# Optimization experiments

Hardware: AMD Instinct MI355X
Metric: run time of the kernel (lower is better)

The kernel has to match this reference:

```python
import jax, jax.numpy as jnp
import numpy as np
import math

EMSIZE = 1024
B, S = 4, 1024
N = B * S

def setup_inputs() -> dict:
    key = jax.random.key(0)
    k1, k2, k3, k4, k5 = jax.random.split(key, 5)
    x = jax.random.normal(k1, (B, S, EMSIZE), dtype=jnp.float32)
    mask = jax.random.randint(k2, (N, N), 0, 2, dtype=jnp.int32)
    # nn.Linear default init scale ~ 1/sqrt(fan_in); use small normal weights
    sc = 1.0 / math.sqrt(EMSIZE)
    Wq = jax.random.normal(k3, (EMSIZE, EMSIZE), dtype=jnp.float32) * sc
    Wk = jax.random.normal(k4, (EMSIZE, EMSIZE), dtype=jnp.float32) * sc
    Wv = jax.random.normal(k5, (EMSIZE, EMSIZE), dtype=jnp.float32) * sc
    return {"x": x, "mask": mask, "Wq": Wq, "Wk": Wk, "Wv": Wv}

def reference(x, mask, Wq, Wk, Wv):
    b, s, e = x.shape
    xf = x.reshape(b * s, e)                       # [N, E]
    q = xf @ Wq.T                                  # nn.Linear: x @ W^T
    k = xf @ Wk.T
    v = xf @ Wv.T
    sim = q @ k.T                                  # [N, N] full cross-batch scores
    sim = jnp.where(mask == 0, jnp.float32(-1e20), sim)
    # NOTE: original scales AFTER masking, matching masked_fill then divide
    attn = jax.nn.softmax(sim / math.sqrt(e), axis=-1)
    out = attn @ v                                 # [N, E]
    return out.reshape(b, s, e)
```

## Files before the change

kernel.cpp:

```cpp
#include <hip/hip_runtime.h>
#include <hip/hip_bf16.h>
#include <math.h>


typedef __attribute__((ext_vector_type(8))) __bf16 bf16x8;
typedef __attribute__((ext_vector_type(4))) __bf16 bf16x4;
typedef __attribute__((ext_vector_type(4))) float f32x4;

__device__ __forceinline__ void gload_lds16(const void* g, void* l) {
  __builtin_amdgcn_global_load_lds(
      (__attribute__((address_space(1))) void*)(g),
      (__attribute__((address_space(3))) void*)(l), 16, 0, 0);
}

#define WAITB(N) asm volatile("s_waitcnt vmcnt(" #N ")\ns_barrier" ::: "memory")

#define LDS_FRAG(base, r) \
  *(const bf16x8*)((base) + (r) * 32 + (((hi) ^ (((r) >> 1) & 3)) * 8))

#define MM16(mq, AF)                                                        \
  __builtin_amdgcn_s_setprio(1);                                            \
  _Pragma("unroll") for (int m = 0; m < 4; ++m)                             \
    _Pragma("unroll") for (int n = 0; n < 4; ++n)                           \
      acc[(mq) * 4 + m][n] = __builtin_amdgcn_mfma_f32_16x16x32_bf16(       \
          AF[m], bfr[n], acc[(mq) * 4 + m][n], 0, 0, 0);                    \
  __builtin_amdgcn_s_setprio(0);

template <int NT>
__device__ __forceinline__ void g8_loop(const __bf16* __restrict__ A, long lda, long row0,
                                        const __bf16* __restrict__ B, long ldb, long col0,
                                        int kt0, __bf16* sA, __bf16* sB,
                                        f32x4 (&acc)[8][4], int tid) {
  const int lane = tid & 63;
  const int w = tid >> 6;
  const int wr = w >> 2, wc = w & 3;
  const int lo = lane & 15, hi = lane >> 4;

  auto stageA = [&](int buf, int kt) {
#pragma unroll
    for (int j = 0; j < 2; ++j) {
      int p = tid + j * 512;
      int row = p >> 2, cg = (p & 3) ^ ((row >> 1) & 3);
      gload_lds16(A + (row0 + row) * lda + kt * 32 + cg * 8,
                  sA + buf * 8192 + p * 8);
    }
  };
  auto stageB = [&](int buf, int kt) {
#pragma unroll
    for (int j = 0; j < 2; ++j) {
      int p = tid + j * 512;
      int row = p >> 2, cg = (p & 3) ^ ((row >> 1) & 3);
      gload_lds16(B + (col0 + row) * ldb + kt * 32 + cg * 8,
                  sB + buf * 8192 + p * 8);
    }
  };

#pragma unroll
  for (int t = 0; t < 3; ++t) { stageA(t, kt0 + t); stageB(t, kt0 + t); }
  WAITB(8);

  for (int t = 0; t < NT; ++t) {
    const int d = t & 3;
    const __bf16* sAc = sA + d * 8192;
    const __bf16* sBc = sB + d * 8192;
    const int s = (t + 3) & 3;
    bf16x8 af[4], bfr[4];
#pragma unroll
    for (int m = 0; m < 4; ++m) af[m] = LDS_FRAG(sAc, wr * 128 + m * 16 + lo);
#pragma unroll
    for (int n = 0; n < 4; ++n) bfr[n] = LDS_FRAG(sBc, wc * 64 + n * 16 + lo);
    if (t + 3 < NT) stageA(s, kt0 + t + 3);
    __builtin_amdgcn_s_barrier();
    MM16(0, af);
    __builtin_amdgcn_s_barrier();
    bf16x8 af2[4];
#pragma unroll
    for (int m = 0; m < 4; ++m) af2[m] = LDS_FRAG(sAc, wr * 128 + 64 + m * 16 + lo);
    if (t + 3 < NT) stageB(s, kt0 + t + 3);
    __builtin_amdgcn_s_barrier();
    MM16(1, af2);
    if (t + 3 < NT)      { WAITB(8); }
    else if (t + 2 < NT) { WAITB(4); }
    else                 { WAITB(0); }
  }
}


__global__ __launch_bounds__(512) void qkv8(const __bf16* __restrict__ xb,
                                            const __bf16* __restrict__ wq,
                                            const __bf16* __restrict__ wk,
                                            const __bf16* __restrict__ wv,
                                            __bf16* __restrict__ qb,
                                            __bf16* __restrict__ kb,
                                            __bf16* __restrict__ vtb) {
  __shared__ __bf16 sA[4 * 8192];
  __shared__ __bf16 sB[4 * 8192];
  const int raw = blockIdx.x;
  const int wid = (raw & 7) * 24 + (raw >> 3);
  const int z = wid >> 6;
  const int r2 = wid & 63;
  const int tid = threadIdx.x;
  const __bf16* A;
  const __bf16* B;
  long row0, col0;
  if (z == 2) {
    A = wv; B = xb;
    row0 = (long)(r2 >> 4) * 256;
    col0 = (long)(r2 & 15) * 256;
  } else {
    A = xb; B = (z == 0) ? wq : wk;
    row0 = (long)(r2 >> 2) * 256;
    col0 = (long)(r2 & 3) * 256;
  }
  f32x4 acc[8][4] = {};
  g8_loop<32>(A, 1024, row0, B, 1024, col0, 0, sA, sB, acc, tid);

  const int lane = tid & 63, w = tid >> 6;
  const int wr = w >> 2, wc = w & 3;
  const int lo = lane & 15, hi = lane >> 4;
#pragma unroll
  for (int m = 0; m < 8; ++m)
#pragma unroll
    for (int n = 0; n < 4; ++n)
#pragma unroll
      for (int i = 0; i < 4; ++i) {
        long r = row0 + wr * 128 + m * 16 + hi * 4 + i;
        long c = col0 + wc * 64 + n * 16 + lo;
        __bf16 v = (__bf16)acc[m][n][i];
        if (z == 0)      qb[r * 1024 + c] = v;
        else if (z == 1) kb[r * 1024 + c] = v;
        else             vtb[r * 4096 + c] = v;
      }
}

__global__ __launch_bounds__(512) void qk8(const __bf16* __restrict__ qb,
                                           const __bf16* __restrict__ kb,
                                           __bf16* __restrict__ sim) {
  __shared__ __bf16 sA[4 * 8192];
  __shared__ __bf16 sB[4 * 8192];
  const int raw = blockIdx.x;
  const int xcd = raw & 7, idx = raw >> 3;
  const int rp = (xcd >> 1) * 4 + (idx >> 3);
  const int cp = (xcd & 1) * 8 + (idx & 7);
  const long row0 = (long)rp * 256;
  const long col0 = (long)cp * 256;
  const int tid = threadIdx.x;
  f32x4 acc[8][4] = {};
  g8_loop<32>(qb, 1024, row0, kb, 1024, col0, 0, sA, sB, acc, tid);

  const int lane = tid & 63, w = tid >> 6;
  const int wr = w >> 2, wc = w & 3;
  const int lo = lane & 15, hi = lane >> 4;
#pragma unroll
  for (int m = 0; m < 8; ++m)
#pragma unroll
    for (int n = 0; n < 4; ++n)
#pragma unroll
      for (int i = 0; i < 4; ++i) {
        long r = row0 + wr * 128 + m * 16 + hi * 4 + i;
        long c = col0 + wc * 64 + n * 16 + lo;
        sim[r * 4096 + c] = (__bf16)acc[m][n][i];
      }
}

__global__ __launch_bounds__(256) void pv4(const __bf16* __restrict__ attn,
                                           const __bf16* __restrict__ vt,
                                           float* __restrict__ out) {
  __shared__ __bf16 sA[4 * 4096];
  __shared__ __bf16 sB[4 * 4096];
  const int raw = blockIdx.x;
  const int xcd = raw & 7, idx = raw >> 3;
  const int rp = (xcd >> 1) * 8 + (idx >> 2);
  const int cp = (xcd & 1) * 4 + (idx & 3);
  const long row0 = (long)rp * 128;
  const long col0 = (long)cp * 128;
  const int tid = threadIdx.x;
  const int lane = tid & 63, w = tid >> 6;
  const int wr = w >> 1, wc = w & 1;
  const int lo = lane & 15, hi = lane >> 4;
  constexpr int NT = 128;

  auto stageA = [&](int buf, int kt) {
#pragma unroll
    for (int j = 0; j < 2; ++j) {
      int p = tid + j * 256;
      int row = p >> 2, cg = (p & 3) ^ ((row >> 1) & 3);
      gload_lds16(attn + (row0 + row) * 4096 + kt * 32 + cg * 8,
                  sA + buf * 4096 + p * 8);
    }
  };
  auto stageB = [&](int buf, int kt) {
#pragma unroll
    for (int j = 0; j < 2; ++j) {
      int p = tid + j * 256;
      int row = p >> 2, cg = (p & 3) ^ ((row >> 1) & 3);
      gload_lds16(vt + (col0 + row) * 4096 + kt * 32 + cg * 8,
                  sB + buf * 4096 + p * 8);
    }
  };

  f32x4 acc[4][4] = {};
#pragma unroll
  for (int t = 0; t < 3; ++t) { stageA(t, t); stageB(t, t); }
  WAITB(8);

#pragma unroll 4
  for (int t = 0; t < NT; ++t) {
    const int d = t & 3;
    const __bf16* sAc = sA + d * 4096;
    const __bf16* sBc = sB + d * 4096;
    const int s = (t + 3) & 3;
    bf16x8 af[4], bfr[4];
#pragma unroll
    for (int m = 0; m < 4; ++m) af[m] = LDS_FRAG(sAc, wr * 64 + m * 16 + lo);
#pragma unroll
    for (int n = 0; n < 4; ++n) bfr[n] = LDS_FRAG(sBc, wc * 64 + n * 16 + lo);
    if (t + 3 < NT) { stageA(s, t + 3); stageB(s, t + 3); }
    __builtin_amdgcn_s_barrier();
    __builtin_amdgcn_s_setprio(1);
#pragma unroll
    for (int m = 0; m < 4; ++m)
#pragma unroll
      for (int n = 0; n < 4; ++n)
        acc[m][n] = __builtin_amdgcn_mfma_f32_16x16x32_bf16(af[m], bfr[n], acc[m][n], 0, 0, 0);
    __builtin_amdgcn_s_setprio(0);
    if (t + 3 < NT)      { WAITB(8); }
    else if (t + 2 < NT) { WAITB(4); }
    else                 { WAITB(0); }
  }

#pragma unroll
  for (int m = 0; m < 4; ++m)
#pragma unroll
    for (int n = 0; n < 4; ++n)
#pragma unroll
      for (int i = 0; i < 4; ++i) {
        long r = row0 + wr * 64 + m * 16 + hi * 4 + i;
        long c = col0 + wc * 64 + n * 16 + lo;
        out[r * 1024 + c] = acc[m][n][i];
      }
}

__global__ __launch_bounds__(256) void softmax_rows(__bf16* __restrict__ sim,
                                                    const int* __restrict__ mask) {
  const int row = blockIdx.x;
  __bf16* rp = sim + (size_t)row * 4096;
  const int4* mrow = (const int4*)(mask + (size_t)row * 4096);
  const int tid = threadIdx.x;

  float vals[16];
  float lmax = -INFINITY;
#pragma unroll
  for (int j = 0; j < 2; ++j) {
    bf16x8 s = ((const bf16x8*)rp)[tid + 256 * j];
    int4 m0 = mrow[(tid + 256 * j) * 2];
    int4 m1 = mrow[(tid + 256 * j) * 2 + 1];
    float f[8];
#pragma unroll
    for (int e = 0; e < 8; ++e) f[e] = (float)s[e];
    f[0] = m0.x ? f[0] : -1e20f;  f[1] = m0.y ? f[1] : -1e20f;
    f[2] = m0.z ? f[2] : -1e20f;  f[3] = m0.w ? f[3] : -1e20f;
    f[4] = m1.x ? f[4] : -1e20f;  f[5] = m1.y ? f[5] : -1e20f;
    f[6] = m1.z ? f[6] : -1e20f;  f[7] = m1.w ? f[7] : -1e20f;
#pragma unroll
    for (int e = 0; e < 8; ++e) {
      vals[8 * j + e] = f[e];
      lmax = fmaxf(lmax, f[e]);
    }
  }
#pragma unroll
  for (int off = 32; off; off >>= 1) lmax = fmaxf(lmax, __shfl_xor(lmax, off));
  __shared__ float red[4];
  __shared__ float bro[2];
  if ((tid & 63) == 0) red[tid >> 6] = lmax;
  __syncthreads();
  if (tid == 0) bro[0] = fmaxf(fmaxf(red[0], red[1]), fmaxf(red[2], red[3]));
  __syncthreads();
  const float m = bro[0];

  float e[16];
  float lsum = 0.f;
#pragma unroll
  for (int j = 0; j < 16; ++j) {
    e[j] = __expf((vals[j] - m) * 0.03125f);
    lsum += e[j];
  }
#pragma unroll
  for (int off = 32; off; off >>= 1) lsum += __shfl_xor(lsum, off);
  if ((tid & 63) == 0) red[tid >> 6] = lsum;
  __syncthreads();
  if (tid == 0) bro[1] = red[0] + red[1] + red[2] + red[3];
  __syncthreads();
  const float inv = 1.0f / bro[1];

#pragma unroll
  for (int j = 0; j < 2; ++j) {
    bf16x8 o;
#pragma unroll
    for (int q = 0; q < 8; ++q) o[q] = (__bf16)(e[8 * j + q] * inv);
    ((bf16x8*)rp)[tid + 256 * j] = o;
  }
}

__global__ __launch_bounds__(256) void cvt_all(const float* __restrict__ x,
                                               const float* __restrict__ wq,
                                               const float* __restrict__ wk,
                                               const float* __restrict__ wv,
                                               __bf16* __restrict__ xb,
                                               __bf16* __restrict__ wqb,
                                               __bf16* __restrict__ wkb,
                                               __bf16* __restrict__ wvb) {
  int b = blockIdx.x;
  const float* in;
  __bf16* out;
  int base;
  if (b < 4096)      { in = x;  out = xb;  base = b; }
  else if (b < 5120) { in = wq; out = wqb; base = b - 4096; }
  else if (b < 6144) { in = wk; out = wkb; base = b - 5120; }
  else               { in = wv; out = wvb; base = b - 6144; }
  int i = base * 256 + threadIdx.x;
  float4 f = ((const float4*)in)[i];
  bf16x4 o;
  o[0] = (__bf16)f.x; o[1] = (__bf16)f.y; o[2] = (__bf16)f.z; o[3] = (__bf16)f.w;
  ((bf16x4*)out)[i] = o;
}

extern "C" void kernel_launch(void* const* d_in, const int* in_sizes, int n_in,
                              void* d_out, int out_size, void* d_ws, size_t ws_size,
                              hipStream_t stream) {
  const float* x = (const float*)d_in[0];
  const int* mask = (const int*)d_in[1];
  const float* Wq = (const float*)d_in[2];
  const float* Wk = (const float*)d_in[3];
  const float* Wv = (const float*)d_in[4];
  float* out = (float*)d_out;

  char* ws = (char*)d_ws;
  __bf16* vtb = (__bf16*)(ws);
  __bf16* xb  = (__bf16*)(ws + (8ull << 20));
  __bf16* wqb = (__bf16*)(ws + (16ull << 20));
  __bf16* wkb = (__bf16*)(ws + (18ull << 20));
  __bf16* wvb = (__bf16*)(ws + (20ull << 20));
  __bf16* qb  = (__bf16*)(ws + (22ull << 20));
  __bf16* kb  = (__bf16*)(ws + (30ull << 20));
  __bf16* sim = (__bf16*)(ws + (38ull << 20));

  cvt_all<<<7168, 256, 0, stream>>>(x, Wq, Wk, Wv, xb, wqb, wkb, wvb);

  qkv8<<<192, 512, 0, stream>>>(xb, wqb, wkb, wvb, qb, kb, vtb);
  qk8<<<256, 512, 0, stream>>>(qb, kb, sim);
  softmax_rows<<<4096, 256, 0, stream>>>(sim, mask);
  pv4<<<256, 256, 0, stream>>>(sim, vtb, out);
}
```

Measured before the change: 155.4 us.

## Split-K the PV GEMM into two halves and add a reduction kernel

The attention-times-V GEMM now launches 512 blocks, each covering half of the 4096-long K dimension. One half writes into the output and the other into a workspace buffer, and a new float4 kernel then adds the two together. The aim is to fill more CUs on a machine with 256 CUs, where the old 256-block grid gave only one wave of blocks. The cost is an extra kernel launch plus 16 MB of fp32 partial-sum traffic. The QK block-to-XCD mapping is also changed, and the unroll pragma on the PV loop is removed.

```diff
diff --git a/kernel.cpp b/kernel.cpp
--- a/kernel.cpp
+++ b/kernel.cpp
@@ -139,11 +139,9 @@
   __shared__ __bf16 sA[4 * 8192];
   __shared__ __bf16 sB[4 * 8192];
   const int raw = blockIdx.x;
-  const int xcd = raw & 7, idx = raw >> 3;
-  const int rp = (xcd >> 1) * 4 + (idx >> 3);
-  const int cp = (xcd & 1) * 8 + (idx & 7);
-  const long row0 = (long)rp * 256;
-  const long col0 = (long)cp * 256;
+  const int wid = (raw & 7) * 32 + (raw >> 3);
+  const long row0 = (long)(wid >> 4) * 256;
+  const long col0 = (long)(wid & 15) * 256;
   const int tid = threadIdx.x;
   f32x4 acc[8][4] = {};
   g8_loop<32>(qb, 1024, row0, kb, 1024, col0, 0, sA, sB, acc, tid);
@@ -165,20 +163,23 @@
 
 __global__ __launch_bounds__(256) void pv4(const __bf16* __restrict__ attn,
                                            const __bf16* __restrict__ vt,
-                                           float* __restrict__ out) {
+                                           float* __restrict__ out,
+                                           float* __restrict__ p1) {
   __shared__ __bf16 sA[4 * 4096];
   __shared__ __bf16 sB[4 * 4096];
   const int raw = blockIdx.x;
-  const int xcd = raw & 7, idx = raw >> 3;
-  const int rp = (xcd >> 1) * 8 + (idx >> 2);
-  const int cp = (xcd & 1) * 4 + (idx & 3);
-  const long row0 = (long)rp * 128;
-  const long col0 = (long)cp * 128;
+  const int wid = (raw & 7) * 64 + (raw >> 3);
+  const int z = wid >> 8;
+  const int r2 = wid & 255;
+  const long row0 = (long)(r2 >> 3) * 128;
+  const long col0 = (long)(r2 & 7) * 128;
+  float* C = z ? p1 : out;
+  const int kt0 = z * 64;
   const int tid = threadIdx.x;
   const int lane = tid & 63, w = tid >> 6;
   const int wr = w >> 1, wc = w & 1;
   const int lo = lane & 15, hi = lane >> 4;
-  constexpr int NT = 128;
+  constexpr int NT = 64;
 
   auto stageA = [&](int buf, int kt) {
 #pragma unroll
@@ -201,10 +202,9 @@
 
   f32x4 acc[4][4] = {};
 #pragma unroll
-  for (int t = 0; t < 3; ++t) { stageA(t, t); stageB(t, t); }
+  for (int t = 0; t < 3; ++t) { stageA(t, kt0 + t); stageB(t, kt0 + t); }
   WAITB(8);
 
-#pragma unroll 4
   for (int t = 0; t < NT; ++t) {
     const int d = t & 3;
     const __bf16* sAc = sA + d * 4096;
@@ -215,7 +215,7 @@
     for (int m = 0; m < 4; ++m) af[m] = LDS_FRAG(sAc, wr * 64 + m * 16 + lo);
 #pragma unroll
     for (int n = 0; n < 4; ++n) bfr[n] = LDS_FRAG(sBc, wc * 64 + n * 16 + lo);
-    if (t + 3 < NT) { stageA(s, t + 3); stageB(s, t + 3); }
+    if (t + 3 < NT) { stageA(s, kt0 + t + 3); stageB(s, kt0 + t + 3); }
     __builtin_amdgcn_s_barrier();
     __builtin_amdgcn_s_setprio(1);
 #pragma unroll
@@ -237,8 +237,17 @@
       for (int i = 0; i < 4; ++i) {
         long r = row0 + wr * 64 + m * 16 + hi * 4 + i;
         long c = col0 + wc * 64 + n * 16 + lo;
-        out[r * 1024 + c] = acc[m][n][i];
+        C[r * 1024 + c] = acc[m][n][i];
       }
+}
+
+__global__ __launch_bounds__(256) void reduce_add2(float* __restrict__ out,
+                                                   const float* __restrict__ p1) {
+  int i = blockIdx.x * 256 + threadIdx.x;
+  float4 a = ((const float4*)out)[i];
+  float4 b = ((const float4*)p1)[i];
+  a.x += b.x; a.y += b.y; a.z += b.z; a.w += b.w;
+  ((float4*)out)[i] = a;
 }
 
 __global__ __launch_bounds__(256) void softmax_rows(__bf16* __restrict__ sim,
@@ -344,11 +353,13 @@
   __bf16* qb  = (__bf16*)(ws + (22ull << 20));
   __bf16* kb  = (__bf16*)(ws + (30ull << 20));
   __bf16* sim = (__bf16*)(ws + (38ull << 20));
+  float*  p1  = (float*)(ws + (8ull << 20));
 
   cvt_all<<<7168, 256, 0, stream>>>(x, Wq, Wk, Wv, xb, wqb, wkb, wvb);
 
   qkv8<<<192, 512, 0, stream>>>(xb, wqb, wkb, wvb, qb, kb, vtb);
   qk8<<<256, 512, 0, stream>>>(qb, kb, sim);
   softmax_rows<<<4096, 256, 0, stream>>>(sim, mask);
-  pv4<<<256, 256, 0, stream>>>(sim, vtb, out);
-}
+  pv4<<<512, 256, 0, stream>>>(sim, vtb, out, p1);
+  reduce_add2<<<4096, 256, 0, stream>>>(out, p1);
+}
```

Result: no change. 154.4 us (-0.7%).
